# Kernel tuning notes

Measured on AMD Instinct MI355X. Metric: run time of the kernel, lower is better.

Reference implementation:

```python
import jax, jax.numpy as jnp
import numpy as np
import math

N = 2_000_000
NUM_LEVELS = 16
MIN_RES, MAX_RES = 16, 2048
FEAT = 2
GROWTH = math.exp((math.log(MAX_RES) - math.log(MIN_RES)) / (NUM_LEVELS - 1))
RES = np.array([int(MIN_RES * GROWTH ** i) for i in range(NUM_LEVELS)], dtype=np.int32)
# Source bug (replicated faithfully): hash is taken mod len(hash_tables[0].weight) = min(16**3, 2**19) = 4096 for ALL levels.
HASH_MOD = min(MIN_RES ** 3, 2 ** 19)  # 4096
PRIMES_MOD = np.array([1 % HASH_MOD, 2654435761 % HASH_MOD, 805459861 % HASH_MOD], dtype=np.int32)
HID, GEO, HIDC, APP = 64, 15, 64, 32


def _lin(key, fin, fout):
    k1, k2 = jax.random.split(key)
    return (jax.random.normal(k1, (fin, fout), jnp.float32) * 0.05,
            jax.random.normal(k2, (fout,), jnp.float32) * 0.01)


def setup_inputs() -> dict:
    key = jax.random.key(0)
    ks = jax.random.split(key, 16)
    inp = {}
    inp['ray_samples'] = jax.random.normal(ks[0], (N, 3), jnp.float32)
    inp['directions'] = jax.random.normal(ks[1], (N, 3), jnp.float32)
    inp['camera_indices'] = jax.random.randint(ks[2], (N,), 0, 1000, jnp.int32)
    inp['aabb'] = jnp.array([[-1.0, -1.0, -1.0], [1.0, 1.0, 1.0]], jnp.float32)
    # hash tables: only first HASH_MOD rows are reachable (source mod bug); init uniform(-1e-4, 1e-4)
    inp['hash_tables'] = jax.random.uniform(ks[3], (NUM_LEVELS, HASH_MOD, FEAT), jnp.float32, -1e-4, 1e-4)
    inp['dir_w1'], inp['dir_b1'] = _lin(ks[4], 3, 16)
    inp['dir_w2'], inp['dir_b2'] = _lin(ks[5], 16, 16)
    inp['dens_w1'], inp['dens_b1'] = _lin(ks[6], NUM_LEVELS * FEAT, HID)
    inp['dens_w2'], inp['dens_b2'] = _lin(ks[7], HID, HID)
    inp['dens_w3'], inp['dens_b3'] = _lin(ks[8], HID, 1 + GEO)
    cin = GEO + 16 + APP  # 63
    inp['col_w1'], inp['col_b1'] = _lin(ks[9], cin, HIDC)
    inp['col_w2'], inp['col_b2'] = _lin(ks[10], HIDC, HIDC)
    inp['col_w3'], inp['col_b3'] = _lin(ks[11], HIDC, 3)
    inp['app_emb'] = jax.random.normal(ks[12], (1000, APP), jnp.float32) * 0.01
    return inp


def hash_encode(positions, hash_tables):
    # positions: [N,3] in [0,1]; hash_tables: [L, HASH_MOD, FEAT]
    res = jnp.asarray(RES)  # [L]
    scaled = positions[None, :, :] * (res[:, None, None] - 1).astype(jnp.float32)  # [L,N,3]
    coords = jnp.clip(jnp.floor(scaled).astype(jnp.int32), 0, res[:, None, None] - 1)
    # (coords * primes).sum(-1) % HASH_MOD, computed mod-safe in int32
    h = (coords * jnp.asarray(PRIMES_MOD)).sum(-1) % HASH_MOD  # [L,N]
    feats = hash_tables[jnp.arange(NUM_LEVELS)[:, None], h]  # [L,N,FEAT] (no trilinear interp, per source)
    return jnp.transpose(feats, (1, 0, 2)).reshape(positions.shape[0], NUM_LEVELS * FEAT)  # [N,32]


def reference(ray_samples, directions, camera_indices, aabb, hash_tables,
              dir_w1, dir_b1, dir_w2, dir_b2,
              dens_w1, dens_b1, dens_w2, dens_b2, dens_w3, dens_b3,
              col_w1, col_b1, col_w2, col_b2, col_w3, col_b3, app_emb):
    positions = jnp.clip((ray_samples - aabb[0]) / (aabb[1] - aabb[0]), 0.0, 1.0)
    enc = hash_encode(positions, hash_tables)  # [N,32]
    h = jax.nn.relu(enc @ dens_w1 + dens_b1)
    h = jax.nn.relu(h @ dens_w2 + dens_b2)
    dfeat = h @ dens_w3 + dens_b3  # [N,16]
    density = jax.nn.relu(dfeat[:, :1])
    geo = dfeat[:, 1:]
    edir = jax.nn.relu(directions @ dir_w1 + dir_b1) @ dir_w2 + dir_b2  # [N,16]
    cin = jnp.concatenate([geo, edir, app_emb[camera_indices]], axis=-1)  # [N,63]
    c = jax.nn.relu(cin @ col_w1 + col_b1)
    c = jax.nn.relu(c @ col_w2 + col_b2)
    rgb = jax.nn.sigmoid(c @ col_w3 + col_b3)  # [N,3]
    return jnp.concatenate([rgb, density, geo], axis=-1)  # [N,19]
```

## Files before the change

kernel.cpp:

```cpp
#include <hip/hip_runtime.h>
#include <math.h>


typedef short short8 __attribute__((ext_vector_type(8)));
typedef float f32x4 __attribute__((ext_vector_type(4)));
typedef unsigned int uint;
typedef unsigned short ushort;

struct EncC { float rf[16]; };

#define PY 2481
#define PZ 1941

#define MFMA(A,B,C) __builtin_amdgcn_mfma_f32_16x16x32_bf16(A, B, C, 0, 0, 0)

#define W1_OFF   0
#define W3_OFF   5120
#define C3_OFF   7424
#define DB1_OFF  9728
#define DB2_OFF  9984
#define DB3_OFF  10240
#define CB1_OFF  10304
#define CB2_OFF  10560
#define CB3_OFF  10816
#define W2_OFF   10848
#define C1_OFF   20064
#define C2_OFF   29280
#define ACT_OFF  10848
#define LDS_BYTES 47712

__device__ __forceinline__ uint bf16rne(float x) {
    uint u = __builtin_bit_cast(uint, x);
    return (u + 0x7fffu + ((u >> 16) & 1u)) >> 16;
}
__device__ __forceinline__ uint packbf(float lo, float hi) {
    return bf16rne(lo) | (bf16rne(hi) << 16);
}

__device__ __forceinline__ void layer_wb(const f32x4* acc, const char* biasp,
                                         char* rowp, int q) {
#pragma unroll
    for (int mt = 0; mt < 4; ++mt) {
        f32x4 bb = *(const f32x4*)(biasp + mt*64 + q*16);
        f32x4 v = acc[mt] + bb;
        uint2 pw;
        pw.x = packbf(fmaxf(v[0], 0.f), fmaxf(v[1], 0.f));
        pw.y = packbf(fmaxf(v[2], 0.f), fmaxf(v[3], 0.f));
        *(uint2*)(rowp + (mt*16 + q*4)*2) = pw;
    }
}

__device__ __forceinline__ void layer64(char* wact, const short8* aw,
                                        const char* biasp, int l15, int q) {
    const int q16 = q * 16;
#pragma unroll
    for (int nt = 0; nt < 4; ++nt) {
        char* rowp = wact + (nt*16 + l15)*144;
        short8 b0 = *(const short8*)(rowp + q16);
        short8 b1 = *(const short8*)(rowp + 64 + q16);
        f32x4 acc[4];
#pragma unroll
        for (int mt = 0; mt < 4; ++mt) {
            f32x4 z = {0.f, 0.f, 0.f, 0.f};
            z = MFMA(aw[2*mt], b0, z);
            acc[mt] = MFMA(aw[2*mt + 1], b1, z);
        }
        layer_wb(acc, biasp, rowp, q);
    }
}

__global__ __launch_bounds__(256, 2)
void nerf_mfma(const float* __restrict__ ray, const float* __restrict__ dirs,
               const int* __restrict__ cam_idx, const float* __restrict__ aabb,
               const float* __restrict__ ht,
               const float* __restrict__ dir_w1, const float* __restrict__ dir_b1,
               const float* __restrict__ dir_w2, const float* __restrict__ dir_b2,
               const float* __restrict__ dens_w1, const float* __restrict__ dens_b1,
               const float* __restrict__ dens_w2, const float* __restrict__ dens_b2,
               const float* __restrict__ dens_w3, const float* __restrict__ dens_b3,
               const float* __restrict__ col_w1, const float* __restrict__ col_b1,
               const float* __restrict__ col_w2, const float* __restrict__ col_b2,
               const float* __restrict__ col_w3, const float* __restrict__ col_b3,
               const float* __restrict__ app_emb,
               float* __restrict__ out, int n, EncC enc)
{
    __shared__ __align__(16) char smem[LDS_BYTES];
    const int t = threadIdx.x;

    {
        uint* z = (uint*)smem;
        for (int i = t; i < 38496/4; i += 256) z[i] = 0;
    }
    __syncthreads();
    {
        ushort* w1t = (ushort*)(smem + W1_OFF);
        for (int e = t; e < 2048; e += 256) w1t[(e&63)*40 + (e>>6)] = (ushort)bf16rne(dens_w1[e]);
        ushort* w2t = (ushort*)(smem + W2_OFF);
        for (int e = t; e < 4096; e += 256) w2t[(e&63)*72 + (e>>6)] = (ushort)bf16rne(dens_w2[e]);
        ushort* w3t = (ushort*)(smem + W3_OFF);
        for (int e = t; e < 1024; e += 256) w3t[(e&15)*72 + (e>>4)] = (ushort)bf16rne(dens_w3[e]);
        ushort* c1t = (ushort*)(smem + C1_OFF);
        for (int e = t; e < 4032; e += 256) {
            int in = e >> 6, o = e & 63;
            int pk = (in < 15) ? (in + 49) : ((in < 31) ? (in + 17) : (in - 31));
            c1t[o*72 + pk] = (ushort)bf16rne(col_w1[e]);
        }
        ushort* c2t = (ushort*)(smem + C2_OFF);
        for (int e = t; e < 4096; e += 256) c2t[(e&63)*72 + (e>>6)] = (ushort)bf16rne(col_w2[e]);
        ushort* c3t = (ushort*)(smem + C3_OFF);
        for (int e = t; e < 192; e += 256) c3t[(e%3)*72 + (e/3)] = (ushort)bf16rne(col_w3[e]);
        if (t < 64) {
            *(float*)(smem + DB1_OFF + t*4) = dens_b1[t];
            *(float*)(smem + DB2_OFF + t*4) = dens_b2[t];
            *(float*)(smem + CB1_OFF + t*4) = col_b1[t];
            *(float*)(smem + CB2_OFF + t*4) = col_b2[t];
        }
        if (t < 16) *(float*)(smem + DB3_OFF + t*4) = dens_b3[t];
        if (t < 4)  *(float*)(smem + CB3_OFF + t*4) = (t < 3) ? col_b3[t] : 0.f;
    }
    __syncthreads();

    const int w = t >> 6, lane = t & 63, l15 = lane & 15, q = lane >> 4;
    const int q16 = q * 16;
    char* wact = smem + ACT_OFF + w*9216;

    short8 aD2[8], aC1[8], aC2[8];
#pragma unroll
    for (int mt = 0; mt < 4; ++mt)
#pragma unroll
        for (int kk = 0; kk < 2; ++kk) {
            const int ro = (mt*16 + l15)*144 + kk*64 + q16;
            aD2[mt*2+kk] = *(const short8*)(smem + W2_OFF + ro);
            aC1[mt*2+kk] = *(const short8*)(smem + C1_OFF + ro);
            aC2[mt*2+kk] = *(const short8*)(smem + C2_OFF + ro);
        }
    __syncthreads();

    const float a0x = aabb[0], a0y = aabb[1], a0z = aabb[2];
    const float ivx = 1.f/(aabb[3]-a0x), ivy = 1.f/(aabb[4]-a0y), ivz = 1.f/(aabb[5]-a0z);

    const int ntiles = (n + 255) >> 8;
    for (int tile = blockIdx.x; tile < ntiles; tile += gridDim.x) {
        const int base = tile*256 + w*64;
        if (base >= n) continue;
        const int s  = base + lane;
        const int sc = min(s, n - 1);

        float px = fminf(fmaxf((ray[3*sc  ] - a0x)*ivx, 0.f), 1.f);
        float py = fminf(fmaxf((ray[3*sc+1] - a0y)*ivy, 0.f), 1.f);
        float pz = fminf(fmaxf((ray[3*sc+2] - a0z)*ivz, 0.f), 1.f);
        uint encp[16];
#pragma unroll
        for (int l = 0; l < 16; ++l) {
            const float rf = enc.rf[l];
            const int cx = (int)(px*rf), cy = (int)(py*rf), cz = (int)(pz*rf);
            const int h = (cx + cy*PY + cz*PZ) & 4095;
            const float2 f = *(const float2*)(ht + (((l<<12) + h) << 1));
            encp[l] = packbf(f.x, f.y);
        }
        uint4* arow = (uint4*)(wact + lane*144);
        arow[0] = make_uint4(encp[0],  encp[1],  encp[2],  encp[3]);
        arow[1] = make_uint4(encp[4],  encp[5],  encp[6],  encp[7]);
        arow[2] = make_uint4(encp[8],  encp[9],  encp[10], encp[11]);
        arow[3] = make_uint4(encp[12], encp[13], encp[14], encp[15]);

        {
            short8 a1[4];
#pragma unroll
            for (int mt = 0; mt < 4; ++mt)
                a1[mt] = *(const short8*)(smem + W1_OFF + (mt*16 + l15)*80 + q16);
#pragma unroll
            for (int nt = 0; nt < 4; ++nt) {
                char* rowp = wact + (nt*16 + l15)*144;
                short8 b = *(const short8*)(rowp + q16);
                f32x4 acc[4];
#pragma unroll
                for (int mt = 0; mt < 4; ++mt) {
                    f32x4 z = {0.f, 0.f, 0.f, 0.f};
                    acc[mt] = MFMA(a1[mt], b, z);
                }
                layer_wb(acc, smem + DB1_OFF, rowp, q);
            }
        }
        layer64(wact, aD2, smem + DB2_OFF, l15, q);
        {
            short8 a0 = *(const short8*)(smem + W3_OFF + l15*144 + q16);
            short8 a1 = *(const short8*)(smem + W3_OFF + l15*144 + 64 + q16);
            f32x4 bb3 = *(const f32x4*)(smem + DB3_OFF + q16);
#pragma unroll
            for (int nt = 0; nt < 4; ++nt) {
                char* rowp = wact + (nt*16 + l15)*144;
                short8 b0 = *(const short8*)(rowp + q16);
                short8 b1 = *(const short8*)(rowp + 64 + q16);
                f32x4 z = {0.f, 0.f, 0.f, 0.f};
                z = MFMA(a0, b0, z);
                f32x4 v = MFMA(a1, b1, z);
                v = v + bb3;
                const int sg = base + nt*16 + l15;
                if (sg < n) {
                    float* op = out + (size_t)sg*19 + 3 + q*4;
                    op[0] = (q == 0) ? fmaxf(v[0], 0.f) : v[0];
                    op[1] = v[1];
                    op[2] = v[2];
                    op[3] = v[3];
                }
                if (q == 0) {
                    *(ushort*)(rowp + 98)  = (ushort)bf16rne(v[1]);
                    *(uint*)  (rowp + 100) = packbf(v[2], v[3]);
                } else {
                    uint2 g;
                    g.x = packbf(v[0], v[1]);
                    g.y = packbf(v[2], v[3]);
                    *(uint2*)(rowp + 96 + 8*q) = g;
                }
            }
        }
        {
            const float dx = dirs[3*sc], dy = dirs[3*sc+1], dz = dirs[3*sc+2];
            float e1[16];
#pragma unroll
            for (int j = 0; j < 16; ++j)
                e1[j] = fmaxf(fmaf(dx, dir_w1[j],
                              fmaf(dy, dir_w1[16+j],
                              fmaf(dz, dir_w1[32+j], dir_b1[j]))), 0.f);
            float ed[16];
#pragma unroll
            for (int j = 0; j < 16; ++j) ed[j] = dir_b2[j];
#pragma unroll
            for (int i = 0; i < 16; ++i) {
                const float e = e1[i];
#pragma unroll
                for (int j = 0; j < 16; ++j) ed[j] = fmaf(e, dir_w2[i*16+j], ed[j]);
            }
            const int cam = cam_idx[sc];
            const float4* ap = (const float4*)(app_emb + (size_t)cam*32);
            uint pk[16];
#pragma unroll
            for (int qd = 0; qd < 8; ++qd) {
                const float4 vv = ap[qd];
                pk[2*qd]   = packbf(vv.x, vv.y);
                pk[2*qd+1] = packbf(vv.z, vv.w);
            }
            arow[0] = make_uint4(pk[0],  pk[1],  pk[2],  pk[3]);
            arow[1] = make_uint4(pk[4],  pk[5],  pk[6],  pk[7]);
            arow[2] = make_uint4(pk[8],  pk[9],  pk[10], pk[11]);
            arow[3] = make_uint4(pk[12], pk[13], pk[14], pk[15]);
            uint ep[8];
#pragma unroll
            for (int j = 0; j < 8; ++j) ep[j] = packbf(ed[2*j], ed[2*j+1]);
            arow[4] = make_uint4(ep[0], ep[1], ep[2], ep[3]);
            arow[5] = make_uint4(ep[4], ep[5], ep[6], ep[7]);
            *(ushort*)(wact + lane*144 + 96) = 0;
        }
        layer64(wact, aC1, smem + CB1_OFF, l15, q);
        layer64(wact, aC2, smem + CB2_OFF, l15, q);
        {
            short8 a0 = *(const short8*)(smem + C3_OFF + l15*144 + q16);
            short8 a1 = *(const short8*)(smem + C3_OFF + l15*144 + 64 + q16);
            f32x4 bbc = *(const f32x4*)(smem + CB3_OFF);
#pragma unroll
            for (int nt = 0; nt < 4; ++nt) {
                char* rowp = wact + (nt*16 + l15)*144;
                short8 b0 = *(const short8*)(rowp + q16);
                short8 b1 = *(const short8*)(rowp + 64 + q16);
                f32x4 z = {0.f, 0.f, 0.f, 0.f};
                z = MFMA(a0, b0, z);
                f32x4 v = MFMA(a1, b1, z);
                const int sg = base + nt*16 + l15;
                if (q == 0 && sg < n) {
                    float* op = out + (size_t)sg*19;
                    op[0] = 1.f / (1.f + __expf(-(v[0] + bbc[0])));
                    op[1] = 1.f / (1.f + __expf(-(v[1] + bbc[1])));
                    op[2] = 1.f / (1.f + __expf(-(v[2] + bbc[2])));
                }
            }
        }
    }
}

extern "C" void kernel_launch(void* const* d_in, const int* in_sizes, int n_in,
                              void* d_out, int out_size, void* d_ws, size_t ws_size,
                              hipStream_t stream)
{
    const float* ray  = (const float*)d_in[0];
    const float* dirs = (const float*)d_in[1];
    const int*   cam  = (const int*)  d_in[2];
    const float* aabb = (const float*)d_in[3];
    const float* ht   = (const float*)d_in[4];
    const float* dw1  = (const float*)d_in[5];
    const float* db1  = (const float*)d_in[6];
    const float* dw2  = (const float*)d_in[7];
    const float* db2  = (const float*)d_in[8];
    const float* nw1  = (const float*)d_in[9];
    const float* nb1  = (const float*)d_in[10];
    const float* nw2  = (const float*)d_in[11];
    const float* nb2  = (const float*)d_in[12];
    const float* nw3  = (const float*)d_in[13];
    const float* nb3  = (const float*)d_in[14];
    const float* cw1  = (const float*)d_in[15];
    const float* cb1  = (const float*)d_in[16];
    const float* cw2  = (const float*)d_in[17];
    const float* cb2  = (const float*)d_in[18];
    const float* cw3  = (const float*)d_in[19];
    const float* cb3  = (const float*)d_in[20];
    const float* app  = (const float*)d_in[21];
    float* out = (float*)d_out;

    const int n = in_sizes[0] / 3;

    EncC enc;
    const double growth = exp((log(2048.0) - log(16.0)) / 15.0);
    for (int i = 0; i < 16; ++i) {
        const int r = (int)(16.0 * pow(growth, (double)i));
        enc.rf[i] = (float)(r - 1);
    }

    const int ntiles = (n + 255) / 256;
    const int grid = ntiles < 512 ? ntiles : 512;
    nerf_mfma<<<grid, 256, 0, stream>>>(
        ray, dirs, cam, aabb, ht,
        dw1, db1, dw2, db2,
        nw1, nb1, nw2, nb2, nw3, nb3,
        cw1, cb1, cw2, cb2, cw3, cb3,
        app, out, n, enc);
}
```

Before: 440.0 us.

## Fold biases into MFMA accumulators, truncate bf16, raise occupancy and vectorize stores

Bias vectors are now used as the initial MFMA accumulator instead of being added after the multiply. bf16 packing switches from round-to-nearest-even to truncation via a single byte-permute instruction. Output stores become vector stores through a per-tile base pointer, with a fast path for full tiles, and the separate zeroing store for the pad slot is replaced by writing zero directly. Launch bounds and grid size are raised from 2 to 3 blocks per CU, which adds register pressure; truncation also slightly changes numerics.

```diff
diff --git a/kernel.cpp b/kernel.cpp
--- a/kernel.cpp
+++ b/kernel.cpp
@@ -4,6 +4,8 @@
 
 typedef short short8 __attribute__((ext_vector_type(8)));
 typedef float f32x4 __attribute__((ext_vector_type(4)));
+typedef float f32x4a __attribute__((ext_vector_type(4), aligned(4)));
+typedef float f32x2a __attribute__((ext_vector_type(2), aligned(4)));
 typedef unsigned int uint;
 typedef unsigned short ushort;
 
@@ -33,26 +35,29 @@
     uint u = __builtin_bit_cast(uint, x);
     return (u + 0x7fffu + ((u >> 16) & 1u)) >> 16;
 }
-__device__ __forceinline__ uint packbf(float lo, float hi) {
-    return bf16rne(lo) | (bf16rne(hi) << 16);
-}
-
-__device__ __forceinline__ void layer_wb(const f32x4* acc, const char* biasp,
-                                         char* rowp, int q) {
+__device__ __forceinline__ uint pktr(float lo, float hi) {
+    return __builtin_amdgcn_perm(__builtin_bit_cast(uint, hi),
+                                 __builtin_bit_cast(uint, lo), 0x07060302u);
+}
+
+__device__ __forceinline__ void layer_wb(const f32x4* acc, char* rowp, int q) {
 #pragma unroll
     for (int mt = 0; mt < 4; ++mt) {
-        f32x4 bb = *(const f32x4*)(biasp + mt*64 + q*16);
-        f32x4 v = acc[mt] + bb;
+        const f32x4 v = acc[mt];
         uint2 pw;
-        pw.x = packbf(fmaxf(v[0], 0.f), fmaxf(v[1], 0.f));
-        pw.y = packbf(fmaxf(v[2], 0.f), fmaxf(v[3], 0.f));
-        *(uint2*)(rowp + (mt*16 + q*4)*2) = pw;
+        pw.x = pktr(fmaxf(v[0], 0.f), fmaxf(v[1], 0.f));
+        pw.y = pktr(fmaxf(v[2], 0.f), fmaxf(v[3], 0.f));
+        *(uint2*)(rowp + mt*32 + q*8) = pw;
     }
 }
 
 __device__ __forceinline__ void layer64(char* wact, const short8* aw,
                                         const char* biasp, int l15, int q) {
     const int q16 = q * 16;
+    f32x4 bf[4];
+#pragma unroll
+    for (int mt = 0; mt < 4; ++mt)
+        bf[mt] = *(const f32x4*)(biasp + mt*64 + q16);
 #pragma unroll
     for (int nt = 0; nt < 4; ++nt) {
         char* rowp = wact + (nt*16 + l15)*144;
@@ -61,15 +66,14 @@
         f32x4 acc[4];
 #pragma unroll
         for (int mt = 0; mt < 4; ++mt) {
-            f32x4 z = {0.f, 0.f, 0.f, 0.f};
-            z = MFMA(aw[2*mt], b0, z);
+            f32x4 z = MFMA(aw[2*mt], b0, bf[mt]);
             acc[mt] = MFMA(aw[2*mt + 1], b1, z);
         }
-        layer_wb(acc, biasp, rowp, q);
-    }
-}
-
-__global__ __launch_bounds__(256, 2)
+        layer_wb(acc, rowp, q);
+    }
+}
+
+__global__ __launch_bounds__(256, 3)
 void nerf_mfma(const float* __restrict__ ray, const float* __restrict__ dirs,
                const int* __restrict__ cam_idx, const float* __restrict__ aabb,
                const float* __restrict__ ht,
@@ -143,8 +147,9 @@
     for (int tile = blockIdx.x; tile < ntiles; tile += gridDim.x) {
         const int base = tile*256 + w*64;
         if (base >= n) continue;
-        const int s  = base + lane;
-        const int sc = min(s, n - 1);
+        const bool full = (base + 64 <= n);
+        const int sc = full ? (base + lane) : min(base + lane, n - 1);
+        float* otile = out + (size_t)base * 19;
 
         float px = fminf(fmaxf((ray[3*sc  ] - a0x)*ivx, 0.f), 1.f);
         float py = fminf(fmaxf((ray[3*sc+1] - a0y)*ivy, 0.f), 1.f);
@@ -156,7 +161,7 @@
             const int cx = (int)(px*rf), cy = (int)(py*rf), cz = (int)(pz*rf);
             const int h = (cx + cy*PY + cz*PZ) & 4095;
             const float2 f = *(const float2*)(ht + (((l<<12) + h) << 1));
-            encp[l] = packbf(f.x, f.y);
+            encp[l] = pktr(f.x, f.y);
         }
         uint4* arow = (uint4*)(wact + lane*144);
         arow[0] = make_uint4(encp[0],  encp[1],  encp[2],  encp[3]);
@@ -166,20 +171,21 @@
 
         {
             short8 a1[4];
-#pragma unroll
-            for (int mt = 0; mt < 4; ++mt)
+            f32x4 bf[4];
+#pragma unroll
+            for (int mt = 0; mt < 4; ++mt) {
                 a1[mt] = *(const short8*)(smem + W1_OFF + (mt*16 + l15)*80 + q16);
+                bf[mt] = *(const f32x4*)(smem + DB1_OFF + mt*64 + q16);
+            }
 #pragma unroll
             for (int nt = 0; nt < 4; ++nt) {
                 char* rowp = wact + (nt*16 + l15)*144;
                 short8 b = *(const short8*)(rowp + q16);
                 f32x4 acc[4];
 #pragma unroll
-                for (int mt = 0; mt < 4; ++mt) {
-                    f32x4 z = {0.f, 0.f, 0.f, 0.f};
-                    acc[mt] = MFMA(a1[mt], b, z);
-                }
-                layer_wb(acc, smem + DB1_OFF, rowp, q);
+                for (int mt = 0; mt < 4; ++mt)
+                    acc[mt] = MFMA(a1[mt], b, bf[mt]);
+                layer_wb(acc, rowp, q);
             }
         }
         layer64(wact, aD2, smem + DB2_OFF, l15, q);
@@ -192,27 +198,16 @@
                 char* rowp = wact + (nt*16 + l15)*144;
                 short8 b0 = *(const short8*)(rowp + q16);
                 short8 b1 = *(const short8*)(rowp + 64 + q16);
-                f32x4 z = {0.f, 0.f, 0.f, 0.f};
-                z = MFMA(a0, b0, z);
+                f32x4 z = MFMA(a0, b0, bb3);
                 f32x4 v = MFMA(a1, b1, z);
-                v = v + bb3;
-                const int sg = base + nt*16 + l15;
-                if (sg < n) {
-                    float* op = out + (size_t)sg*19 + 3 + q*4;
-                    op[0] = (q == 0) ? fmaxf(v[0], 0.f) : v[0];
-                    op[1] = v[1];
-                    op[2] = v[2];
-                    op[3] = v[3];
-                }
-                if (q == 0) {
-                    *(ushort*)(rowp + 98)  = (ushort)bf16rne(v[1]);
-                    *(uint*)  (rowp + 100) = packbf(v[2], v[3]);
-                } else {
-                    uint2 g;
-                    g.x = packbf(v[0], v[1]);
-                    g.y = packbf(v[2], v[3]);
-                    *(uint2*)(rowp + 96 + 8*q) = g;
-                }
+                uint2 g;
+                g.x = pktr(q == 0 ? 0.f : v[0], v[1]);
+                g.y = pktr(v[2], v[3]);
+                *(uint2*)(rowp + 96 + 8*q) = g;
+                if (q == 0) v[0] = fmaxf(v[0], 0.f);
+                const int sg = nt*16 + l15;
+                if (full || base + sg < n)
+                    *(f32x4a*)(otile + sg*19 + 3 + q16/4) = v;
             }
         }
         {
@@ -238,8 +233,8 @@
 #pragma unroll
             for (int qd = 0; qd < 8; ++qd) {
                 const float4 vv = ap[qd];
-                pk[2*qd]   = packbf(vv.x, vv.y);
-                pk[2*qd+1] = packbf(vv.z, vv.w);
+                pk[2*qd]   = pktr(vv.x, vv.y);
+                pk[2*qd+1] = pktr(vv.z, vv.w);
             }
             arow[0] = make_uint4(pk[0],  pk[1],  pk[2],  pk[3]);
             arow[1] = make_uint4(pk[4],  pk[5],  pk[6],  pk[7]);
@@ -247,10 +242,9 @@
             arow[3] = make_uint4(pk[12], pk[13], pk[14], pk[15]);
             uint ep[8];
 #pragma unroll
-            for (int j = 0; j < 8; ++j) ep[j] = packbf(ed[2*j], ed[2*j+1]);
+            for (int j = 0; j < 8; ++j) ep[j] = pktr(ed[2*j], ed[2*j+1]);
             arow[4] = make_uint4(ep[0], ep[1], ep[2], ep[3]);
             arow[5] = make_uint4(ep[4], ep[5], ep[6], ep[7]);
-            *(ushort*)(wact + lane*144 + 96) = 0;
         }
         layer64(wact, aC1, smem + CB1_OFF, l15, q);
         layer64(wact, aC2, smem + CB2_OFF, l15, q);
@@ -263,15 +257,16 @@
                 char* rowp = wact + (nt*16 + l15)*144;
                 short8 b0 = *(const short8*)(rowp + q16);
                 short8 b1 = *(const short8*)(rowp + 64 + q16);
-                f32x4 z = {0.f, 0.f, 0.f, 0.f};
-                z = MFMA(a0, b0, z);
+                f32x4 z = MFMA(a0, b0, bbc);
                 f32x4 v = MFMA(a1, b1, z);
-                const int sg = base + nt*16 + l15;
-                if (q == 0 && sg < n) {
-                    float* op = out + (size_t)sg*19;
-                    op[0] = 1.f / (1.f + __expf(-(v[0] + bbc[0])));
-                    op[1] = 1.f / (1.f + __expf(-(v[1] + bbc[1])));
-                    op[2] = 1.f / (1.f + __expf(-(v[2] + bbc[2])));
+                const int sg = nt*16 + l15;
+                if (q == 0 && (full || base + sg < n)) {
+                    float* op = otile + sg*19;
+                    f32x2a r01;
+                    r01[0] = 1.f / (1.f + __expf(-v[0]));
+                    r01[1] = 1.f / (1.f + __expf(-v[1]));
+                    *(f32x2a*)op = r01;
+                    op[2] = 1.f / (1.f + __expf(-v[2]));
                 }
             }
         }
@@ -316,7 +311,7 @@
     }
 
     const int ntiles = (n + 255) / 256;
-    const int grid = ntiles < 512 ? ntiles : 512;
+    const int grid = ntiles < 768 ? ntiles : 768;
     nerf_mfma<<<grid, 256, 0, stream>>>(
         ray, dirs, cam, aabb, ht,
         dw1, db1, dw2, db2,
```

Result: faster. 418.3 us (-4.9%).
